# Kernel optimization log

Hardware: AMD Instinct MI355X
Metric: run time of the kernel (lower is better)

## Reference

```python
import jax, jax.numpy as jnp
import numpy as np

R = 2_097_152          # rays
M, C = 8, 16           # subjects, channels
TEX_SHAPES = [(M, C, 512, 512), (M, C, 256, 256)]


def setup_inputs() -> dict:
    key = jax.random.key(0)
    k1, k2, k3, k4, k5 = jax.random.split(key, 5)
    uv_coords = jax.random.uniform(k1, (R, 2), jnp.float32) * 2.0 - 1.0   # in [-1,1]
    subject_id = jax.random.uniform(k2, (R,), jnp.float32) * 2.0 - 1.0    # normalized subject coord
    uv_idcs = jax.random.randint(k3, (R,), 0, len(TEX_SHAPES), jnp.int32)
    tex0 = jax.random.normal(k4, TEX_SHAPES[0], jnp.float32)
    tex1 = jax.random.normal(k5, TEX_SHAPES[1], jnp.float32)
    return {"uv_coords": uv_coords, "uv_idcs": uv_idcs, "subject_id": subject_id,
            "tex0": tex0, "tex1": tex1}


def _trilinear_border(tex, u, v, z):
    """Trilinear sample of tex [M,C,H,W] at (x=u->W, y=v->H, z->M),
    matching F.grid_sample(align_corners=True, padding_mode='border').
    u,v,z: [R] in [-1,1]. Returns [R,C]."""
    Mm, Cc, H, W = tex.shape
    t = jnp.transpose(tex, (0, 2, 3, 1))  # [M,H,W,C] for channel-contiguous gathers
    # align_corners=True unnormalization, border clamp
    x = jnp.clip((u + 1.0) * 0.5 * (W - 1), 0.0, W - 1)
    y = jnp.clip((v + 1.0) * 0.5 * (H - 1), 0.0, H - 1)
    d = jnp.clip((z + 1.0) * 0.5 * (Mm - 1), 0.0, Mm - 1)
    x0 = jnp.floor(x).astype(jnp.int32); x1 = jnp.minimum(x0 + 1, W - 1)
    y0 = jnp.floor(y).astype(jnp.int32); y1 = jnp.minimum(y0 + 1, H - 1)
    d0 = jnp.floor(d).astype(jnp.int32); d1 = jnp.minimum(d0 + 1, Mm - 1)
    wx = (x - x0.astype(x.dtype))[:, None]
    wy = (y - y0.astype(y.dtype))[:, None]
    wd = (d - d0.astype(d.dtype))[:, None]

    def g(di, yi, xi):
        return t[di, yi, xi]  # [R,C]

    v00 = g(d0, y0, x0) * (1 - wx) + g(d0, y0, x1) * wx
    v01 = g(d0, y1, x0) * (1 - wx) + g(d0, y1, x1) * wx
    v10 = g(d1, y0, x0) * (1 - wx) + g(d1, y0, x1) * wx
    v11 = g(d1, y1, x0) * (1 - wx) + g(d1, y1, x1) * wx
    v0 = v00 * (1 - wy) + v01 * wy
    v1 = v10 * (1 - wy) + v11 * wy
    return v0 * (1 - wd) + v1 * wd


def reference(uv_coords, uv_idcs, subject_id, tex0, tex1):
    u, v = uv_coords[:, 0], uv_coords[:, 1]
    s0 = _trilinear_border(tex0, u, v, subject_id)  # [R,C]
    s1 = _trilinear_border(tex1, u, v, subject_id)  # [R,C]
    ret = jnp.where((uv_idcs == 0)[:, None], s0, s1)  # route by texture id
    return ret.T  # [C,R]
```

## Files before the change

kernel.cpp:

```cpp
#include <hip/hip_runtime.h>
#include <hip/hip_fp16.h>

#define R_TOTAL 2097152
#define M_DEPTH 8
#define C_CH 16

struct C32 { float4 q[4]; };

__global__ __launch_bounds__(256) void repack_dup_fp16(const float* __restrict__ src,
                                                       __half* __restrict__ dst,
                                                       int lgW) {
    int t = blockIdx.x * blockDim.x + threadIdx.x;
    int W  = 1 << lgW;
    int HW = 1 << (2 * lgW);
    int m  = t >> (2 * lgW);
    int p  = t & (HW - 1);
    int x  = p & (W - 1);
    int x1off = (x == W - 1) ? 0 : 1;

    const float* s = src + (size_t)m * C_CH * HW + p;
    union { __half h[2 * C_CH]; float4 f[4]; } u;
#pragma unroll
    for (int c = 0; c < C_CH; ++c) {
        float a = __builtin_nontemporal_load(s + (size_t)c * HW);
        float b = __builtin_nontemporal_load(s + (size_t)c * HW + x1off);
        u.h[c]        = __float2half(a);
        u.h[C_CH + c] = __float2half(b);
    }
    float4* d4 = (float4*)(dst + (size_t)t * 2 * C_CH);
#pragma unroll
    for (int r = 0; r < 4; ++r) d4[r] = u.f[r];
}

__device__ inline void corner_accum(const C32& c, float w, float wx,
                                    float acc[C_CH]) {
    const __half2* pa = (const __half2*)&c.q[0];
    const __half2* pb = (const __half2*)&c.q[2];
#pragma unroll
    for (int k = 0; k < 8; ++k) {
        float2 fa = __half22float2(pa[k]);
        float2 fb = __half22float2(pb[k]);
        acc[2 * k + 0] += w * (fa.x + wx * (fb.x - fa.x));
        acc[2 * k + 1] += w * (fa.y + wx * (fb.y - fa.y));
    }
}

__global__ __launch_bounds__(256) void sample_dup_fp16(
    const float* __restrict__ uv, const int* __restrict__ idcs,
    const float* __restrict__ sid, const __half* __restrict__ tex0p,
    const __half* __restrict__ tex1p, float* __restrict__ out) {
    int i = blockIdx.x * blockDim.x + threadIdx.x;

    float tu  = __builtin_nontemporal_load(uv + 2 * (size_t)i + 0);
    float tv  = __builtin_nontemporal_load(uv + 2 * (size_t)i + 1);
    float z   = __builtin_nontemporal_load(sid + i);
    int which = __builtin_nontemporal_load(idcs + i);

    const __half* tex = (which == 0) ? tex0p : tex1p;
    int   Wm1 = (which == 0) ? 511 : 255;
    int   W   = Wm1 + 1;
    float fw  = (float)Wm1;

    float x = fminf(fmaxf((tu + 1.0f) * 0.5f * fw, 0.0f), fw);
    float y = fminf(fmaxf((tv + 1.0f) * 0.5f * fw, 0.0f), fw);
    float d = fminf(fmaxf((z + 1.0f) * 0.5f * 7.0f, 0.0f), 7.0f);

    int x0 = (int)x, y0 = (int)y, d0 = (int)d;
    int y1 = min(y0 + 1, Wm1), d1 = min(d0 + 1, 7);
    float wx = x - (float)x0, wy = y - (float)y0, wd = d - (float)d0;

    float w_d[2] = {1.0f - wd, wd};
    float w_y[2] = {1.0f - wy, wy};
    int   ds[2]  = {d0, d1};
    int   ys[2]  = {y0, y1};

    C32 cv[2][2];
#pragma unroll
    for (int a = 0; a < 2; ++a)
#pragma unroll
        for (int b = 0; b < 2; ++b) {
            const C32* e = (const C32*)(tex +
                ((size_t)(ds[a] * W + ys[b]) * W + x0) * (2 * C_CH));
            cv[a][b] = *e;
        }

    float acc[C_CH];
#pragma unroll
    for (int c = 0; c < C_CH; ++c) acc[c] = 0.0f;
#pragma unroll
    for (int a = 0; a < 2; ++a)
#pragma unroll
        for (int b = 0; b < 2; ++b)
            corner_accum(cv[a][b], w_d[a] * w_y[b], wx, acc);

#pragma unroll
    for (int c = 0; c < C_CH; ++c)
        __builtin_nontemporal_store(acc[c], out + (size_t)c * R_TOTAL + i);
}

__global__ __launch_bounds__(256) void repack_f32(const float* __restrict__ src,
                                                  float* __restrict__ dst,
                                                  int lgHW) {
    int t = blockIdx.x * blockDim.x + threadIdx.x;
    int HW = 1 << lgHW;
    int m  = t >> lgHW;
    int p  = t & (HW - 1);
    const float* s = src + (size_t)m * C_CH * HW + p;
    float v[C_CH];
#pragma unroll
    for (int c = 0; c < C_CH; ++c) v[c] = s[(size_t)c * HW];
    float4* d4 = (float4*)(dst + (size_t)t * C_CH);
#pragma unroll
    for (int r = 0; r < 4; ++r)
        d4[r] = make_float4(v[4 * r + 0], v[4 * r + 1], v[4 * r + 2], v[4 * r + 3]);
}

__global__ __launch_bounds__(256) void sample_packed_f32(
    const float2* __restrict__ uv, const int* __restrict__ idcs,
    const float* __restrict__ sid, const float* __restrict__ tex0p,
    const float* __restrict__ tex1p, float* __restrict__ out) {
    int i = blockIdx.x * blockDim.x + threadIdx.x;

    float2 t  = uv[i];
    float  z  = sid[i];
    int which = idcs[i];

    const float* tex = (which == 0) ? tex0p : tex1p;
    int   Wm1 = (which == 0) ? 511 : 255;
    int   W   = Wm1 + 1;
    float fw  = (float)Wm1;

    float x = fminf(fmaxf((t.x + 1.0f) * 0.5f * fw, 0.0f), fw);
    float y = fminf(fmaxf((t.y + 1.0f) * 0.5f * fw, 0.0f), fw);
    float d = fminf(fmaxf((z + 1.0f) * 0.5f * 7.0f, 0.0f), 7.0f);

    int x0 = (int)x, y0 = (int)y, d0 = (int)d;
    int x1 = min(x0 + 1, Wm1), y1 = min(y0 + 1, Wm1), d1 = min(d0 + 1, 7);
    float wx = x - (float)x0, wy = y - (float)y0, wd = d - (float)d0;

    float acc[C_CH];
#pragma unroll
    for (int c = 0; c < C_CH; ++c) acc[c] = 0.0f;

    float w_d[2] = {1.0f - wd, wd};
    float w_y[2] = {1.0f - wy, wy};
    int   ds[2]  = {d0, d1};
    int   ys[2]  = {y0, y1};

#pragma unroll
    for (int a = 0; a < 2; ++a)
#pragma unroll
        for (int b = 0; b < 2; ++b) {
            float w = w_d[a] * w_y[b];
            const float* base = tex + (size_t)(ds[a] * W + ys[b]) * W * C_CH;
            const float4* pa = (const float4*)(base + (size_t)x0 * C_CH);
            const float4* pb = (const float4*)(base + (size_t)x1 * C_CH);
#pragma unroll
            for (int r = 0; r < 4; ++r) {
                float4 va = pa[r];
                float4 vb = pb[r];
                acc[4 * r + 0] += w * (va.x + wx * (vb.x - va.x));
                acc[4 * r + 1] += w * (va.y + wx * (vb.y - va.y));
                acc[4 * r + 2] += w * (va.z + wx * (vb.z - va.z));
                acc[4 * r + 3] += w * (va.w + wx * (vb.w - va.w));
            }
        }

#pragma unroll
    for (int c = 0; c < C_CH; ++c)
        out[(size_t)c * R_TOTAL + i] = acc[c];
}

__global__ __launch_bounds__(256) void sample_direct(
    const float2* __restrict__ uv, const int* __restrict__ idcs,
    const float* __restrict__ sid, const float* __restrict__ tex0,
    const float* __restrict__ tex1, float* __restrict__ out) {
    int i = blockIdx.x * blockDim.x + threadIdx.x;

    float2 t  = uv[i];
    float  z  = sid[i];
    int which = idcs[i];

    const float* tex = (which == 0) ? tex0 : tex1;
    int   Wm1 = (which == 0) ? 511 : 255;
    int   W   = Wm1 + 1;
    float fw  = (float)Wm1;

    float x = fminf(fmaxf((t.x + 1.0f) * 0.5f * fw, 0.0f), fw);
    float y = fminf(fmaxf((t.y + 1.0f) * 0.5f * fw, 0.0f), fw);
    float d = fminf(fmaxf((z + 1.0f) * 0.5f * 7.0f, 0.0f), 7.0f);

    int x0 = (int)x, y0 = (int)y, d0 = (int)d;
    int x1 = min(x0 + 1, Wm1), y1 = min(y0 + 1, Wm1), d1 = min(d0 + 1, 7);
    float wx = x - (float)x0, wy = y - (float)y0, wd = d - (float)d0;

    float w_d[2] = {1.0f - wd, wd};
    float w_y[2] = {1.0f - wy, wy};
    int   ds[2]  = {d0, d1};
    int   ys[2]  = {y0, y1};

#pragma unroll
    for (int c = 0; c < C_CH; ++c) {
        float res = 0.0f;
#pragma unroll
        for (int a = 0; a < 2; ++a)
#pragma unroll
            for (int b = 0; b < 2; ++b) {
                float w = w_d[a] * w_y[b];
                const float* base =
                    tex + ((size_t)ds[a] * C_CH + c) * W * W + (size_t)ys[b] * W;
                float va = base[x0];
                float vb = base[x1];
                res += w * (va + wx * (vb - va));
            }
        out[(size_t)c * R_TOTAL + i] = res;
    }
}

extern "C" void kernel_launch(void* const* d_in, const int* in_sizes, int n_in,
                              void* d_out, int out_size, void* d_ws, size_t ws_size,
                              hipStream_t stream) {
    const float* uv   = (const float*)d_in[0];
    const int*   idcs = (const int*)d_in[1];
    const float* sid  = (const float*)d_in[2];
    const float* tex0 = (const float*)d_in[3];
    const float* tex1 = (const float*)d_in[4];
    float*       out  = (float*)d_out;

    const size_t e0 = (size_t)M_DEPTH * 512 * 512;
    const size_t e1 = (size_t)M_DEPTH * 256 * 256;
    const size_t need_dup = (e0 + e1) * 2 * C_CH * sizeof(__half);
    const size_t need_f32 = (e0 + e1) * C_CH * sizeof(float);

    if (ws_size >= need_dup) {
        __half* p0 = (__half*)d_ws;
        __half* p1 = p0 + e0 * 2 * C_CH;
        repack_dup_fp16<<<(int)(e0 / 256), 256, 0, stream>>>(tex0, p0, 9);
        repack_dup_fp16<<<(int)(e1 / 256), 256, 0, stream>>>(tex1, p1, 8);
        sample_dup_fp16<<<R_TOTAL / 256, 256, 0, stream>>>(uv, idcs, sid, p0, p1, out);
    } else if (ws_size >= need_f32) {
        float* p0 = (float*)d_ws;
        float* p1 = p0 + e0 * C_CH;
        repack_f32<<<(int)(e0 / 256), 256, 0, stream>>>(tex0, p0, 18);
        repack_f32<<<(int)(e1 / 256), 256, 0, stream>>>(tex1, p1, 16);
        sample_packed_f32<<<R_TOTAL / 256, 256, 0, stream>>>((const float2*)uv, idcs, sid,
                                                             p0, p1, out);
    } else {
        sample_direct<<<R_TOTAL / 256, 256, 0, stream>>>((const float2*)uv, idcs, sid,
                                                         tex0, tex1, out);
    }
}
```

Measured before the change: 271.2 us.

## Vectorize texture repack with 4 texels per thread, shuffles and LDS-staged stores

The fp16 duplicate-neighbour repack now handles 4 texels per thread with 16-byte loads. It gets the right neighbour through a wave shuffle instead of a second scalar load, then transposes through shared memory so global stores are fully coalesced. The two per-texture repack launches become a single launch, which saves one launch overhead. The unused f32 fallback path is removed. The change targets the repack's scalar uncoalesced reads and strided writes, at the cost of more LDS use and register pressure.

```diff
diff --git a/kernel.cpp b/kernel.cpp
--- a/kernel.cpp
+++ b/kernel.cpp
@@ -5,31 +5,78 @@
 #define M_DEPTH 8
 #define C_CH 16
 
+typedef float f32x4 __attribute__((ext_vector_type(4)));
+
 struct C32 { float4 q[4]; };
 
-__global__ __launch_bounds__(256) void repack_dup_fp16(const float* __restrict__ src,
-                                                       __half* __restrict__ dst,
-                                                       int lgW) {
-    int t = blockIdx.x * blockDim.x + threadIdx.x;
+#define NG0 (M_DEPTH * 512 * 512 / 4)
+#define NG1 (M_DEPTH * 256 * 256 / 4)
+
+__global__ __launch_bounds__(256) void repack_dup_fp16_v2(
+    const float* __restrict__ src0, __half* __restrict__ dst0,
+    const float* __restrict__ src1, __half* __restrict__ dst1) {
+    __shared__ float4 ls[4 * 17 * 64];
+
+    int t = blockIdx.x * 256 + threadIdx.x;
+    const float* src;
+    __half* dst;
+    int lgW, tg;
+    if (t < NG0) { src = src0; dst = dst0; lgW = 9; tg = t; }
+    else         { src = src1; dst = dst1; lgW = 8; tg = t - NG0; }
+
     int W  = 1 << lgW;
     int HW = 1 << (2 * lgW);
-    int m  = t >> (2 * lgW);
-    int p  = t & (HW - 1);
+    int g  = tg << 2;
+    int m  = g >> (2 * lgW);
+    int p  = g & (HW - 1);
     int x  = p & (W - 1);
-    int x1off = (x == W - 1) ? 0 : 1;
+    int lane = threadIdx.x & 63;
+    int wv   = threadIdx.x >> 6;
 
     const float* s = src + (size_t)m * C_CH * HW + p;
-    union { __half h[2 * C_CH]; float4 f[4]; } u;
-#pragma unroll
-    for (int c = 0; c < C_CH; ++c) {
-        float a = __builtin_nontemporal_load(s + (size_t)c * HW);
-        float b = __builtin_nontemporal_load(s + (size_t)c * HW + x1off);
-        u.h[c]        = __float2half(a);
-        u.h[C_CH + c] = __float2half(b);
-    }
-    float4* d4 = (float4*)(dst + (size_t)t * 2 * C_CH);
-#pragma unroll
-    for (int r = 0; r < 4; ++r) d4[r] = u.f[r];
+
+    f32x4 a[C_CH];
+#pragma unroll
+    for (int c = 0; c < C_CH; ++c)
+        a[c] = __builtin_nontemporal_load((const f32x4*)(s + (size_t)c * HW));
+
+    bool rowend4 = (x == W - 4);
+    float nb[C_CH];
+#pragma unroll
+    for (int c = 0; c < C_CH; ++c) nb[c] = __shfl_down(a[c].x, 1, 64);
+    if (lane == 63 && !rowend4) {
+#pragma unroll
+        for (int c = 0; c < C_CH; ++c)
+            nb[c] = __builtin_nontemporal_load(s + (size_t)c * HW + 4);
+    }
+    if (rowend4) {
+#pragma unroll
+        for (int c = 0; c < C_CH; ++c) nb[c] = a[c].w;
+    }
+
+    float4* lsw = ls + wv * (17 * 64);
+#pragma unroll
+    for (int k = 0; k < 4; ++k) {
+        union { __half h[2 * C_CH]; float4 f[4]; } u;
+#pragma unroll
+        for (int c = 0; c < C_CH; ++c) {
+            u.h[c]        = __float2half(a[c][k]);
+            u.h[C_CH + c] = __float2half(k < 3 ? a[c][k + 1] : nb[c]);
+        }
+#pragma unroll
+        for (int r = 0; r < 4; ++r)
+            lsw[lane * 17 + (k * 4 + r)] = u.f[r];
+    }
+    __syncthreads();
+
+    int tg_w = tg - lane;
+    float4* dst4 = (float4*)dst + (size_t)tg_w * 16;
+#pragma unroll
+    for (int r2 = 0; r2 < 16; ++r2) {
+        int j = r2 * 64 + lane;
+        float4 v = lsw[j + (j >> 4)];
+        dst4[j] = v;
+    }
 }
 
 __device__ inline void corner_accum(const C32& c, float w, float wx,
@@ -96,79 +143,6 @@
 #pragma unroll
     for (int c = 0; c < C_CH; ++c)
         __builtin_nontemporal_store(acc[c], out + (size_t)c * R_TOTAL + i);
-}
-
-__global__ __launch_bounds__(256) void repack_f32(const float* __restrict__ src,
-                                                  float* __restrict__ dst,
-                                                  int lgHW) {
-    int t = blockIdx.x * blockDim.x + threadIdx.x;
-    int HW = 1 << lgHW;
-    int m  = t >> lgHW;
-    int p  = t & (HW - 1);
-    const float* s = src + (size_t)m * C_CH * HW + p;
-    float v[C_CH];
-#pragma unroll
-    for (int c = 0; c < C_CH; ++c) v[c] = s[(size_t)c * HW];
-    float4* d4 = (float4*)(dst + (size_t)t * C_CH);
-#pragma unroll
-    for (int r = 0; r < 4; ++r)
-        d4[r] = make_float4(v[4 * r + 0], v[4 * r + 1], v[4 * r + 2], v[4 * r + 3]);
-}
-
-__global__ __launch_bounds__(256) void sample_packed_f32(
-    const float2* __restrict__ uv, const int* __restrict__ idcs,
-    const float* __restrict__ sid, const float* __restrict__ tex0p,
-    const float* __restrict__ tex1p, float* __restrict__ out) {
-    int i = blockIdx.x * blockDim.x + threadIdx.x;
-
-    float2 t  = uv[i];
-    float  z  = sid[i];
-    int which = idcs[i];
-
-    const float* tex = (which == 0) ? tex0p : tex1p;
-    int   Wm1 = (which == 0) ? 511 : 255;
-    int   W   = Wm1 + 1;
-    float fw  = (float)Wm1;
-
-    float x = fminf(fmaxf((t.x + 1.0f) * 0.5f * fw, 0.0f), fw);
-    float y = fminf(fmaxf((t.y + 1.0f) * 0.5f * fw, 0.0f), fw);
-    float d = fminf(fmaxf((z + 1.0f) * 0.5f * 7.0f, 0.0f), 7.0f);
-
-    int x0 = (int)x, y0 = (int)y, d0 = (int)d;
-    int x1 = min(x0 + 1, Wm1), y1 = min(y0 + 1, Wm1), d1 = min(d0 + 1, 7);
-    float wx = x - (float)x0, wy = y - (float)y0, wd = d - (float)d0;
-
-    float acc[C_CH];
-#pragma unroll
-    for (int c = 0; c < C_CH; ++c) acc[c] = 0.0f;
-
-    float w_d[2] = {1.0f - wd, wd};
-    float w_y[2] = {1.0f - wy, wy};
-    int   ds[2]  = {d0, d1};
-    int   ys[2]  = {y0, y1};
-
-#pragma unroll
-    for (int a = 0; a < 2; ++a)
-#pragma unroll
-        for (int b = 0; b < 2; ++b) {
-            float w = w_d[a] * w_y[b];
-            const float* base = tex + (size_t)(ds[a] * W + ys[b]) * W * C_CH;
-            const float4* pa = (const float4*)(base + (size_t)x0 * C_CH);
-            const float4* pb = (const float4*)(base + (size_t)x1 * C_CH);
-#pragma unroll
-            for (int r = 0; r < 4; ++r) {
-                float4 va = pa[r];
-                float4 vb = pb[r];
-                acc[4 * r + 0] += w * (va.x + wx * (vb.x - va.x));
-                acc[4 * r + 1] += w * (va.y + wx * (vb.y - va.y));
-                acc[4 * r + 2] += w * (va.z + wx * (vb.z - va.z));
-                acc[4 * r + 3] += w * (va.w + wx * (vb.w - va.w));
-            }
-        }
-
-#pragma unroll
-    for (int c = 0; c < C_CH; ++c)
-        out[(size_t)c * R_TOTAL + i] = acc[c];
 }
 
 __global__ __launch_bounds__(256) void sample_direct(
@@ -230,21 +204,12 @@
     const size_t e0 = (size_t)M_DEPTH * 512 * 512;
     const size_t e1 = (size_t)M_DEPTH * 256 * 256;
     const size_t need_dup = (e0 + e1) * 2 * C_CH * sizeof(__half);
-    const size_t need_f32 = (e0 + e1) * C_CH * sizeof(float);
 
     if (ws_size >= need_dup) {
         __half* p0 = (__half*)d_ws;
         __half* p1 = p0 + e0 * 2 * C_CH;
-        repack_dup_fp16<<<(int)(e0 / 256), 256, 0, stream>>>(tex0, p0, 9);
-        repack_dup_fp16<<<(int)(e1 / 256), 256, 0, stream>>>(tex1, p1, 8);
+        repack_dup_fp16_v2<<<(NG0 + NG1) / 256, 256, 0, stream>>>(tex0, p0, tex1, p1);
         sample_dup_fp16<<<R_TOTAL / 256, 256, 0, stream>>>(uv, idcs, sid, p0, p1, out);
-    } else if (ws_size >= need_f32) {
-        float* p0 = (float*)d_ws;
-        float* p1 = p0 + e0 * C_CH;
-        repack_f32<<<(int)(e0 / 256), 256, 0, stream>>>(tex0, p0, 18);
-        repack_f32<<<(int)(e1 / 256), 256, 0, stream>>>(tex1, p1, 16);
-        sample_packed_f32<<<R_TOTAL / 256, 256, 0, stream>>>((const float2*)uv, idcs, sid,
-                                                             p0, p1, out);
     } else {
         sample_direct<<<R_TOTAL / 256, 256, 0, stream>>>((const float2*)uv, idcs, sid,
                                                          tex0, tex1, out);
```

Result: faster. 233.3 us (-14.0%).
